# Kernel optimization log

Hardware: AMD Instinct MI355X
Metric: run time of the kernel (lower is better)

The kernel has to match this reference:

```python
import jax, jax.numpy as jnp
import numpy as np

T, B, N, DEG, F_IN, H, C = 48, 32, 96, 8, 16, 128, 500
E = B * N * DEG          # edges per timestep (already batch-offset within [0, B*N))
M = T * B * N            # total nodes across all timesteps
EPS = 1e-5               # BatchNorm eps


def setup_inputs() -> dict:
    key = jax.random.key(0)
    ks = jax.random.split(key, 24)
    rn = lambda k, s: jax.random.normal(k, s, dtype=jnp.float32) * 0.05
    return {
        "x": jax.random.normal(ks[0], (T, B * N, F_IN), dtype=jnp.float32),
        "edge_index": jax.random.randint(ks[1], (T, 2, E), 0, B * N, dtype=jnp.int32),
        "gcn_w0": rn(ks[2], (F_IN, H)),
        "gcn_w12": rn(ks[3], (2, H, H)),
        "gcn_b": rn(ks[4], (3, H)),
        "bn_gamma": jnp.ones((3, H), dtype=jnp.float32),
        "bn_beta": jnp.zeros((3, H), dtype=jnp.float32),
        "bn_mean": rn(ks[5], (3, H)),
        "bn_var": jax.random.uniform(ks[6], (3, H), minval=0.5, maxval=1.5, dtype=jnp.float32),
        "lstm_wih0": rn(ks[7], (2, 4 * H, H)),
        "lstm_whh0": rn(ks[8], (2, 4 * H, H)),
        "lstm_bih0": rn(ks[9], (2, 4 * H)),
        "lstm_bhh0": rn(ks[10], (2, 4 * H)),
        "lstm_wih1": rn(ks[11], (2, 4 * H, 2 * H)),
        "lstm_whh1": rn(ks[12], (2, 4 * H, H)),
        "lstm_bih1": rn(ks[13], (2, 4 * H)),
        "lstm_bhh1": rn(ks[14], (2, 4 * H)),
        "attn_w1": rn(ks[15], (2 * H, H)),
        "attn_b1": rn(ks[16], (H,)),
        "attn_w2": rn(ks[17], (H, 1)),
        "attn_b2": rn(ks[18], (1,)),
        "fc1_w": rn(ks[19], (2 * H, H)),
        "fc1_b": rn(ks[20], (H,)),
        "fc2_w": rn(ks[21], (H, C)),
        "fc2_b": rn(ks[22], (C,)),
    }


def _lstm_dir(x, wih, whh, bih, bhh):
    # x: [T, B, I]; PyTorch gate order i, f, g, o
    pre = jnp.einsum('tbi,gi->tbg', x, wih) + bih  # input projection hoisted out of scan
    h0 = jnp.zeros((x.shape[1], whh.shape[1]), x.dtype)

    def step(carry, p):
        h, c = carry
        g = p + h @ whh.T + bhh
        i, f, gg, o = jnp.split(g, 4, axis=-1)
        c = jax.nn.sigmoid(f) * c + jax.nn.sigmoid(i) * jnp.tanh(gg)
        h = jax.nn.sigmoid(o) * jnp.tanh(c)
        return (h, c), h

    _, hs = jax.lax.scan(step, (h0, h0), pre)
    return hs  # [T, B, Hh]


def _bilstm(x, wih, whh, bih, bhh):
    fwd = _lstm_dir(x, wih[0], whh[0], bih[0], bhh[0])
    bwd = _lstm_dir(x[::-1], wih[1], whh[1], bih[1], bhh[1])[::-1]
    return jnp.concatenate([fwd, bwd], axis=-1)  # [T, B, 2H]


def reference(x, edge_index, gcn_w0, gcn_w12, gcn_b,
              bn_gamma, bn_beta, bn_mean, bn_var,
              lstm_wih0, lstm_whh0, lstm_bih0, lstm_bhh0,
              lstm_wih1, lstm_whh1, lstm_bih1, lstm_bhh1,
              attn_w1, attn_b1, attn_w2, attn_b2,
              fc1_w, fc1_b, fc2_w, fc2_b):
    # Fold timesteps into one big node set by offsetting indices by t*B*N
    off = (jnp.arange(T, dtype=jnp.int32) * (B * N))[:, None]
    src = (edge_index[:, 0] + off).reshape(-1)
    dst = (edge_index[:, 1] + off).reshape(-1)

    # GCN symmetric norm with self-loops: deg counts incoming edges + self-loop
    deg = jax.ops.segment_sum(jnp.ones_like(src, dtype=x.dtype), dst, num_segments=M) + 1.0
    dinv = jax.lax.rsqrt(deg)
    enorm = (dinv[src] * dinv[dst])[:, None]   # per-edge norm
    self_norm = (1.0 / deg)[:, None]           # self-loop norm

    h = x.reshape(M, F_IN)
    for l in range(3):
        W = gcn_w0 if l == 0 else gcn_w12[l - 1]
        hw = h @ W  # GCNConv applies linear first
        z = jax.ops.segment_sum(hw[src] * enorm, dst, num_segments=M) + hw * self_norm + gcn_b[l]
        # BatchNorm1d eval-mode (running stats), then ReLU, residual if shapes match
        z = (z - bn_mean[l]) * (bn_gamma[l] * jax.lax.rsqrt(bn_var[l] + EPS)) + bn_beta[l]
        z = jax.nn.relu(z)
        h = z + h if l > 0 else z  # dropout is identity in eval

    # global_mean_pool per graph (fixed N nodes per graph)
    emb = h.reshape(T, B, N, H).mean(axis=2)  # [T, B, H]

    out1 = _bilstm(emb, lstm_wih0, lstm_whh0, lstm_bih0, lstm_bhh0)
    out2 = _bilstm(out1, lstm_wih1, lstm_whh1, lstm_bih1, lstm_bhh1)
    lstm_out = out2.transpose(1, 0, 2)  # [B, T, 2H]

    a = jnp.tanh(lstm_out @ attn_w1 + attn_b1) @ attn_w2 + attn_b2  # [B, T, 1]
    w = jax.nn.softmax(a, axis=1)
    ws = jnp.sum(lstm_out * w, axis=1)  # [B, 2H]

    y = jax.nn.relu(ws @ fc1_w + fc1_b) @ fc2_w + fc2_b
    return jax.nn.log_softmax(y, axis=1)
```

## Files before the change

kernel.cpp:

```cpp
#include <hip/hip_runtime.h>

#define T_ 48
#define B_ 32
#define N_ 96
#define E_ 24576
#define BN_ (B_*N_)
#define M_ (T_*BN_)
#define FIN_ 16
#define H_ 128
#define C_ 500
#define TE_ (T_*E_)
#define EPS_ 1e-5f

typedef _Float16 f16x8 __attribute__((ext_vector_type(8)));
typedef float    f32x4 __attribute__((ext_vector_type(4)));
typedef _Float16 half2v __attribute__((ext_vector_type(2)));

__device__ __forceinline__ ushort f2h(float f) {
    _Float16 h = (_Float16)f;
    union { _Float16 h; ushort u; } v;
    v.h = h;
    return v.u;
}
__device__ __forceinline__ float h2f(ushort u) {
    union { ushort u; _Float16 h; } v;
    v.u = u;
    return (float)v.h;
}
__device__ __forceinline__ half2v pkfma(unsigned int v, unsigned int w, half2v acc) {
#if __has_builtin(__builtin_elementwise_fma)
    return __builtin_elementwise_fma(__builtin_bit_cast(half2v, v),
                                     __builtin_bit_cast(half2v, w), acc);
#else
    half2v hv = __builtin_bit_cast(half2v, v);
    half2v wv = __builtin_bit_cast(half2v, w);
    acc[0] += hv[0]*wv[0];
    acc[1] += hv[1]*wv[1];
    return acc;
#endif
}
__device__ __forceinline__ float dot2pk(unsigned int hbits, unsigned int wbits, float acc) {
#if __has_builtin(__builtin_amdgcn_fdot2)
    return __builtin_amdgcn_fdot2(__builtin_bit_cast(half2v, hbits),
                                  __builtin_bit_cast(half2v, wbits), acc, false);
#else
    half2v hv = __builtin_bit_cast(half2v, hbits);
    half2v wv = __builtin_bit_cast(half2v, wbits);
    acc = fmaf((float)hv[0], (float)wv[0], acc);
    acc = fmaf((float)hv[1], (float)wv[1], acc);
    return acc;
#endif
}
__device__ __forceinline__ float sigm(float x) {
    return 1.f / (1.f + __expf(-x));
}
__device__ __forceinline__ float ftanh(float x) {
    x = fminf(15.f, fmaxf(-15.f, x));
    float e = __expf(2.f * x);
    return (e - 1.f) / (e + 1.f);
}

__global__ __launch_bounds__(1024) void csr_build_k(
    const int* __restrict__ ei, int* __restrict__ csr_off,
    unsigned int* __restrict__ csr_pk, float* __restrict__ dinv)
{
    int t = blockIdx.x;
    int tid = threadIdx.x;
    __shared__ int cnt[BN_];
    __shared__ int cur[BN_];
    __shared__ int scanbuf[1024];
    __shared__ unsigned int pk[E_];

    #pragma unroll
    for (int i = 0; i < 3; i++) cnt[tid + i*1024] = 0;
    __syncthreads();

    const int* srcp = ei + ((long)t*2+0)*E_;
    const int* dstp = ei + ((long)t*2+1)*E_;
    #pragma unroll
    for (int i = 0; i < E_/1024; i++)
        atomicAdd(&cnt[dstp[tid + i*1024]], 1);
    __syncthreads();

    int n0 = tid*3;
    int a = cnt[n0], b = cnt[n0+1], c = cnt[n0+2];
    int tot = a + b + c;
    scanbuf[tid] = tot;
    __syncthreads();
    for (int d = 1; d < 1024; d <<= 1) {
        int add = (tid >= d) ? scanbuf[tid-d] : 0;
        __syncthreads();
        scanbuf[tid] += add;
        __syncthreads();
    }
    int excl = scanbuf[tid] - tot;
    cur[n0] = excl; cur[n0+1] = excl + a; cur[n0+2] = excl + a + b;
    int gbase = t*BN_, ebase = t*E_;
    csr_off[gbase+n0]   = ebase + excl;
    csr_off[gbase+n0+1] = ebase + excl + a;
    csr_off[gbase+n0+2] = ebase + excl + a + b;
    dinv[gbase+n0]   = rsqrtf((float)a + 1.f);
    dinv[gbase+n0+1] = rsqrtf((float)b + 1.f);
    dinv[gbase+n0+2] = rsqrtf((float)c + 1.f);
    if (t == T_-1 && tid == 0) csr_off[M_] = TE_;
    __syncthreads();

    #pragma unroll
    for (int i = 0; i < E_/1024; i++) {
        int e = tid + i*1024;
        int s = srcp[e], d = dstp[e];
        int pos = atomicAdd(&cur[d], 1);
        float w = rsqrtf((float)cnt[s] + 1.f) * rsqrtf((float)cnt[d] + 1.f);
        pk[pos] = (unsigned int)s | ((unsigned int)f2h(w) << 16);
    }
    __syncthreads();

    uint4* dpk = (uint4*)(csr_pk + ebase);
    const uint4* spk = (const uint4*)pk;
    #pragma unroll
    for (int i = 0; i < E_/4096; i++)
        dpk[tid + i*1024] = spk[tid + i*1024];
}

#define WPREP_TOTAL (384+1024+4096+16384+16384+65536+65536+131072+262144)
__global__ void wprep_k(
    const float* __restrict__ gcn_b, const float* __restrict__ gam,
    const float* __restrict__ bet, const float* __restrict__ mu,
    const float* __restrict__ var,
    float* __restrict__ bn_sc, float* __restrict__ bn_sh,
    const float* __restrict__ bih0, const float* __restrict__ bhh0,
    float* __restrict__ bias0,
    const float* __restrict__ bih1, const float* __restrict__ bhh1,
    float* __restrict__ bias1,
    const float* __restrict__ gcn_w0, const float* __restrict__ gcn_w12,
    ushort* __restrict__ w0t, ushort* __restrict__ w1t, ushort* __restrict__ w2t,
    const float* __restrict__ whh0, const float* __restrict__ whh1,
    unsigned int* __restrict__ wpk0, unsigned int* __restrict__ wpk1,
    const float* __restrict__ wih0, const float* __restrict__ wih1,
    ushort* __restrict__ wih0b, ushort* __restrict__ wih1b)
{
    int i = blockIdx.x * blockDim.x + threadIdx.x;
    if (i >= WPREP_TOTAL) return;
    if (i < 384) {
        float sc = gam[i] * rsqrtf(var[i] + EPS_);
        bn_sc[i] = sc;
        bn_sh[i] = gcn_b[i]*sc + bet[i] - mu[i]*sc;
        return;
    }
    i -= 384;
    if (i < 1024) {
        bias0[i] = bih0[i] + bhh0[i];
        bias1[i] = bih1[i] + bhh1[i];
        return;
    }
    i -= 1024;
    if (i < 4096) {
        int e = i & 7, lane = (i >> 3) & 63, ct = i >> 9;
        int k = (lane >> 4)*8 + e;
        int c = ct*16 + (lane & 15);
        w0t[i] = (k < 16) ? f2h(gcn_w0[k*128 + c]) : (ushort)0;
        return;
    }
    i -= 4096;
    if (i < 16384) {
        int e = i & 7, lane = (i >> 3) & 63, kk = (i >> 9) & 3, ct = i >> 11;
        int k = kk*32 + (lane >> 4)*8 + e;
        int c = ct*16 + (lane & 15);
        w1t[i] = f2h(gcn_w12[k*128 + c]);
        return;
    }
    i -= 16384;
    if (i < 16384) {
        int e = i & 7, lane = (i >> 3) & 63, kk = (i >> 9) & 3, ct = i >> 11;
        int k = kk*32 + (lane >> 4)*8 + e;
        int c = ct*16 + (lane & 15);
        w2t[i] = f2h(gcn_w12[16384 + k*128 + c]);
        return;
    }
    i -= 16384;
    if (i < 65536) {
        int dir = i >> 15, r = i & 32767;
        int ab = r >> 14, r2 = r & 16383;
        int q = r2 >> 8, tidw = r2 & 255;
        int hh = tidw >> 1, gp = tidw & 1;
        int g = (2*gp + ab)*128 + hh;
        const float* wr = whh0 + ((long)(dir*512 + g))*128 + 2*q;
        wpk0[i] = (unsigned int)f2h(wr[0]) | ((unsigned int)f2h(wr[1]) << 16);
        return;
    }
    i -= 65536;
    if (i < 65536) {
        int dir = i >> 15, r = i & 32767;
        int ab = r >> 14, r2 = r & 16383;
        int q = r2 >> 8, tidw = r2 & 255;
        int hh = tidw >> 1, gp = tidw & 1;
        int g = (2*gp + ab)*128 + hh;
        const float* wr = whh1 + ((long)(dir*512 + g))*128 + 2*q;
        wpk1[i] = (unsigned int)f2h(wr[0]) | ((unsigned int)f2h(wr[1]) << 16);
        return;
    }
    i -= 65536;
    if (i < 131072) {
        int dir = i >> 16, r = i & 0xFFFF;
        int nt = r >> 11, kk = (r >> 9) & 3, lane = (r >> 3) & 63, e = r & 7;
        int n = nt*16 + (lane & 15);
        int k = kk*32 + (lane >> 4)*8 + e;
        wih0b[i] = f2h(wih0[((long)dir*512 + n)*128 + k]);
        return;
    }
    i -= 131072;
    {
        int dir = i >> 17, r = i & 0x1FFFF;
        int nt = r >> 12, kk = (r >> 9) & 7, lane = (r >> 3) & 63, e = r & 7;
        int n = nt*16 + (lane & 15);
        int k = kk*32 + (lane >> 4)*8 + e;
        wih1b[i] = f2h(wih1[((long)dir*512 + n)*256 + k]);
    }
}


__global__ __launch_bounds__(256) void gather128_k(
    const ushort* __restrict__ h, ushort* __restrict__ out,
    const int* __restrict__ csr_off, const unsigned int* __restrict__ csr_pk,
    const float* __restrict__ dinv)
{
    int nb = gridDim.x;
    int chunk = nb >> 3;
    int bswz = (blockIdx.x & 7) * chunk + (blockIdx.x >> 3);
    int wv = threadIdx.x >> 6;
    int nodeA = __builtin_amdgcn_readfirstlane(bswz*8 + wv*2);
    int tbase = (nodeA / BN_) * BN_;
    int lane = threadIdx.x & 63;
    int l2 = lane * 2;
    int e00 = __builtin_amdgcn_readfirstlane(csr_off[nodeA]);
    int e01 = __builtin_amdgcn_readfirstlane(csr_off[nodeA+1]);
    int e11 = __builtin_amdgcn_readfirstlane(csr_off[nodeA+2]);
    int dA = e01 - e00, dB = e11 - e01;
    unsigned int mypkA = (lane < dA) ? csr_pk[e00 + lane] : 0u;
    unsigned int mypkB = (lane < dB) ? csr_pk[e01 + lane] : 0u;
    float dvA = dinv[nodeA], dvB = dinv[nodeA+1];
    unsigned int selfA = *(const unsigned int*)(h + (size_t)nodeA*128 + l2);
    unsigned int selfB = *(const unsigned int*)(h + (size_t)(nodeA+1)*128 + l2);

    ushort swA = f2h(dvA * dvA), swB = f2h(dvB * dvB);
    half2v spA = __builtin_bit_cast(half2v, (unsigned int)(swA * 0x10001u));
    half2v spB = __builtin_bit_cast(half2v, (unsigned int)(swB * 0x10001u));
    half2v a0 = __builtin_bit_cast(half2v, selfA);
    a0[0] *= spA[0]; a0[1] *= spA[1];
    half2v b0 = __builtin_bit_cast(half2v, selfB);
    b0[0] *= spB[0]; b0[1] *= spB[1];
    half2v a1 = {(_Float16)0.f, (_Float16)0.f}, a2 = a1, a3 = a1;
    half2v b1 = a1, b2 = a1, b3 = a1;

    int cA = (dA < 64) ? dA : 64;
    int cB = (dB < 64) ? dB : 64;
    int cA4 = cA & ~3, cB4 = cB & ~3;
    int cm = (cA4 > cB4) ? cA4 : cB4;
    for (int j = 0; j < cm; j += 4) {
        unsigned int pA0, pA1, pA2, pA3, vA0, vA1, vA2, vA3;
        unsigned int pB0, pB1, pB2, pB3, vB0, vB1, vB2, vB3;
        bool qA = (j < cA4), qB = (j < cB4);
        if (qA) {
            pA0 = (unsigned int)__builtin_amdgcn_readlane((int)mypkA, j+0);
            pA1 = (unsigned int)__builtin_amdgcn_readlane((int)mypkA, j+1);
            pA2 = (unsigned int)__builtin_amdgcn_readlane((int)mypkA, j+2);
            pA3 = (unsigned int)__builtin_amdgcn_readlane((int)mypkA, j+3);
            vA0 = *(const unsigned int*)(h + (size_t)(tbase + (int)(pA0 & 0xffffu))*128 + l2);
            vA1 = *(const unsigned int*)(h + (size_t)(tbase + (int)(pA1 & 0xffffu))*128 + l2);
            vA2 = *(const unsigned int*)(h + (size_t)(tbase + (int)(pA2 & 0xffffu))*128 + l2);
            vA3 = *(const unsigned int*)(h + (size_t)(tbase + (int)(pA3 & 0xffffu))*128 + l2);
        }
        if (qB) {
            pB0 = (unsigned int)__builtin_amdgcn_readlane((int)mypkB, j+0);
            pB1 = (unsigned int)__builtin_amdgcn_readlane((int)mypkB, j+1);
            pB2 = (unsigned int)__builtin_amdgcn_readlane((int)mypkB, j+2);
            pB3 = (unsigned int)__builtin_amdgcn_readlane((int)mypkB, j+3);
            vB0 = *(const unsigned int*)(h + (size_t)(tbase + (int)(pB0 & 0xffffu))*128 + l2);
            vB1 = *(const unsigned int*)(h + (size_t)(tbase + (int)(pB1 & 0xffffu))*128 + l2);
            vB2 = *(const unsigned int*)(h + (size_t)(tbase + (int)(pB2 & 0xffffu))*128 + l2);
            vB3 = *(const unsigned int*)(h + (size_t)(tbase + (int)(pB3 & 0xffffu))*128 + l2);
        }
        if (qA) {
            a0 = pkfma(vA0, (pA0 >> 16) * 0x10001u, a0);
            a1 = pkfma(vA1, (pA1 >> 16) * 0x10001u, a1);
            a2 = pkfma(vA2, (pA2 >> 16) * 0x10001u, a2);
            a3 = pkfma(vA3, (pA3 >> 16) * 0x10001u, a3);
        }
        if (qB) {
            b0 = pkfma(vB0, (pB0 >> 16) * 0x10001u, b0);
            b1 = pkfma(vB1, (pB1 >> 16) * 0x10001u, b1);
            b2 = pkfma(vB2, (pB2 >> 16) * 0x10001u, b2);
            b3 = pkfma(vB3, (pB3 >> 16) * 0x10001u, b3);
        }
    }
    for (int j = cA4; j < cA; j++) {
        unsigned int pk0 = (unsigned int)__builtin_amdgcn_readlane((int)mypkA, j);
        unsigned int v = *(const unsigned int*)(h + (size_t)(tbase + (int)(pk0 & 0xffffu))*128 + l2);
        a0 = pkfma(v, (pk0 >> 16) * 0x10001u, a0);
    }
    for (int j = cB4; j < cB; j++) {
        unsigned int pk0 = (unsigned int)__builtin_amdgcn_readlane((int)mypkB, j);
        unsigned int v = *(const unsigned int*)(h + (size_t)(tbase + (int)(pk0 & 0xffffu))*128 + l2);
        b0 = pkfma(v, (pk0 >> 16) * 0x10001u, b0);
    }
    for (int jj = e00 + 64; jj < e01; jj++) {
        unsigned int pk0 = __builtin_amdgcn_readfirstlane(csr_pk[jj]);
        unsigned int v = *(const unsigned int*)(h + (size_t)(tbase + (int)(pk0 & 0xffffu))*128 + l2);
        a0 = pkfma(v, (pk0 >> 16) * 0x10001u, a0);
    }
    for (int jj = e01 + 64; jj < e11; jj++) {
        unsigned int pk0 = __builtin_amdgcn_readfirstlane(csr_pk[jj]);
        unsigned int v = *(const unsigned int*)(h + (size_t)(tbase + (int)(pk0 & 0xffffu))*128 + l2);
        b0 = pkfma(v, (pk0 >> 16) * 0x10001u, b0);
    }
    float ra0 = ((float)a0[0] + (float)a1[0]) + ((float)a2[0] + (float)a3[0]);
    float ra1 = ((float)a0[1] + (float)a1[1]) + ((float)a2[1] + (float)a3[1]);
    float rb0 = ((float)b0[0] + (float)b1[0]) + ((float)b2[0] + (float)b3[0]);
    float rb1 = ((float)b0[1] + (float)b1[1]) + ((float)b2[1] + (float)b3[1]);
    *(unsigned int*)(out + (size_t)nodeA*128 + l2) =
        (unsigned int)f2h(ra0) | ((unsigned int)f2h(ra1) << 16);
    *(unsigned int*)(out + (size_t)(nodeA+1)*128 + l2) =
        (unsigned int)f2h(rb0) | ((unsigned int)f2h(rb1) << 16);
}

__global__ __launch_bounds__(256) void gcn0_k(
    const float* __restrict__ x, const ushort* __restrict__ Wt,
    ushort* __restrict__ Cout,
    const int* __restrict__ csr_off, const unsigned int* __restrict__ csr_pk,
    const float* __restrict__ dinv,
    const float* __restrict__ bnsc, const float* __restrict__ bnsh)
{
    __shared__ ushort agg[64][32];
    __shared__ ushort cl[64][136];
    int tid = threadIdx.x;
    int nl = tid >> 2;
    int fq = tid & 3;
    int f0 = fq*4;
    int node = blockIdx.x*64 + nl;
    int tbase = (node / BN_) * BN_;
    float dv = dinv[node];
    float4 sv = *(const float4*)(x + (long)node*16 + f0);
    float s = dv*dv;
    float a0 = sv.x*s, a1 = sv.y*s, a2 = sv.z*s, a3 = sv.w*s;
    int e0 = csr_off[node], e1 = csr_off[node+1];
    int j = e0;
    for (; j + 4 <= e1; j += 4) {
        unsigned int p0 = csr_pk[j], p1 = csr_pk[j+1], p2 = csr_pk[j+2], p3 = csr_pk[j+3];
        int s0 = tbase + (int)(p0 & 0xffffu), s1 = tbase + (int)(p1 & 0xffffu);
        int s2 = tbase + (int)(p2 & 0xffffu), s3 = tbase + (int)(p3 & 0xffffu);
        float w0 = h2f((ushort)(p0 >> 16)), w1 = h2f((ushort)(p1 >> 16));
        float w2 = h2f((ushort)(p2 >> 16)), w3 = h2f((ushort)(p3 >> 16));
        float4 v0 = *(const float4*)(x + (long)s0*16 + f0);
        float4 v1 = *(const float4*)(x + (long)s1*16 + f0);
        float4 v2 = *(const float4*)(x + (long)s2*16 + f0);
        float4 v3 = *(const float4*)(x + (long)s3*16 + f0);
        a0 += v0.x*w0 + v1.x*w1 + v2.x*w2 + v3.x*w3;
        a1 += v0.y*w0 + v1.y*w1 + v2.y*w2 + v3.y*w3;
        a2 += v0.z*w0 + v1.z*w1 + v2.z*w2 + v3.z*w3;
        a3 += v0.w*w0 + v1.w*w1 + v2.w*w2 + v3.w*w3;
    }
    for (; j < e1; j++) {
        unsigned int pk0 = csr_pk[j];
        int sc = tbase + (int)(pk0 & 0xffffu);
        float en = h2f((ushort)(pk0 >> 16));
        float4 v = *(const float4*)(x + (long)sc*16 + f0);
        a0 += v.x*en; a1 += v.y*en; a2 += v.z*en; a3 += v.w*en;
    }
    agg[nl][f0+0] = f2h(a0);
    agg[nl][f0+1] = f2h(a1);
    agg[nl][f0+2] = f2h(a2);
    agg[nl][f0+3] = f2h(a3);
    agg[nl][16+f0+0] = 0;
    agg[nl][16+f0+1] = 0;
    agg[nl][16+f0+2] = 0;
    agg[nl][16+f0+3] = 0;
    __syncthreads();

    int w = tid >> 6, lane = tid & 63;
    int l16 = lane & 15, lh = lane >> 4;
    f16x8 af = *reinterpret_cast<const f16x8*>(&agg[w*16 + l16][lh*8]);
    f32x4 acc[8];
    #pragma unroll
    for (int i = 0; i < 8; i++) acc[i] = (f32x4){0.f, 0.f, 0.f, 0.f};
    #pragma unroll
    for (int ct = 0; ct < 8; ct++) {
        f16x8 bfr = *reinterpret_cast<const f16x8*>(&Wt[((long)ct*64 + lane)*8]);
        acc[ct] = __builtin_amdgcn_mfma_f32_16x16x32_f16(af, bfr, acc[ct], 0, 0, 0);
    }

    #pragma unroll
    for (int ct = 0; ct < 8; ct++) {
        int col = ct*16 + l16;
        float sc = bnsc[col], sh = bnsh[col];
        #pragma unroll
        for (int r = 0; r < 4; r++) {
            int rl = w*16 + lh*4 + r;
            float v = acc[ct][r] * sc + sh;
            cl[rl][col] = f2h(fmaxf(v, 0.f));
        }
    }
    __syncthreads();
    long rowblock = (long)blockIdx.x * 64;
    #pragma unroll
    for (int it = 0; it < 4; it++) {
        int ss = it*256 + tid;
        int rl = ss >> 4, c8 = (ss & 15) * 8;
        uint4 v = *(const uint4*)&cl[rl][c8];
        *(uint4*)&Cout[(rowblock + rl)*128 + c8] = v;
    }
}

template<int K, bool HASRES>
__global__ __launch_bounds__(256) void mm_mfma_k(
    const ushort* __restrict__ A, const ushort* __restrict__ Wt,
    ushort* __restrict__ Cout,
    const float* __restrict__ bnsc, const float* __restrict__ bnsh,
    const ushort* __restrict__ resid)
{
    constexpr int KST = (K >= 32) ? (K/32) : 1;
    int tid = threadIdx.x;
    int w = tid >> 6, lane = tid & 63;
    int l16 = lane & 15, lh = lane >> 4;
    int row0 = blockIdx.x * 64 + w * 16;
    __shared__ ushort cl[64][136];

    f32x4 acc[8];
    #pragma unroll
    for (int i = 0; i < 8; i++) acc[i] = (f32x4){0.f, 0.f, 0.f, 0.f};

    #pragma unroll
    for (int kk = 0; kk < KST; kk++) {
        int ka = kk*32 + lh*8;
        f16x8 af;
        bool valid = (K >= 32) || (ka < K);
        if (valid) {
            af = *reinterpret_cast<const f16x8*>(&A[(long)(row0 + l16)*K + ka]);
        } else {
            #pragma unroll
            for (int e = 0; e < 8; e++) af[e] = (_Float16)0.f;
        }
        #pragma unroll
        for (int ct = 0; ct < 8; ct++) {
            f16x8 bfr = *reinterpret_cast<const f16x8*>(
                &Wt[(((long)ct*KST + kk)*64 + lane)*8]);
            acc[ct] = __builtin_amdgcn_mfma_f32_16x16x32_f16(af, bfr, acc[ct], 0, 0, 0);
        }
    }

    #pragma unroll
    for (int ct = 0; ct < 8; ct++) {
        int col = ct*16 + l16;
        float sc = bnsc[col], sh = bnsh[col];
        #pragma unroll
        for (int r = 0; r < 4; r++) {
            int rl = w*16 + lh*4 + r;
            float v = acc[ct][r] * sc + sh;
            cl[rl][col] = f2h(fmaxf(v, 0.f));
        }
    }
    __syncthreads();
    long rowblock = (long)blockIdx.x * 64;
    #pragma unroll
    for (int it = 0; it < 4; it++) {
        int s = it*256 + tid;
        int rl = s >> 4, c8 = (s & 15) * 8;
        uint4 v = *(const uint4*)&cl[rl][c8];
        if (HASRES) {
            uint4 rv = *(const uint4*)&resid[(rowblock + rl)*128 + c8];
            half2v* vv = (half2v*)&v;
            const half2v* rr = (const half2v*)&rv;
            vv[0] += rr[0]; vv[1] += rr[1]; vv[2] += rr[2]; vv[3] += rr[3];
        }
        *(uint4*)&Cout[(rowblock + rl)*128 + c8] = v;
    }
}

template<int K>
__global__ __launch_bounds__(256) void mm_pre_k(
    const ushort* __restrict__ A, const ushort* __restrict__ Wt_all,
    float* __restrict__ Cout_all, const float* __restrict__ bias_all)
{
    constexpr int KST = K/32;
    int dir = blockIdx.z;
    const ushort* Wt = Wt_all + (size_t)dir * 512 * K;
    float* Cout = Cout_all + (size_t)dir * T_ * B_ * 512;
    const float* bias = bias_all + dir * 512;

    int tid = threadIdx.x;
    int w = tid >> 6, lane = tid & 63;
    int l16 = lane & 15, lh = lane >> 4;
    int row0 = blockIdx.x * 64 + w * 16;
    int nt0 = blockIdx.y * 8;

    f32x4 acc[8];
    #pragma unroll
    for (int i = 0; i < 8; i++) acc[i] = (f32x4){0.f, 0.f, 0.f, 0.f};

    #pragma unroll
    for (int kk = 0; kk < KST; kk++) {
        int ka = kk*32 + lh*8;
        f16x8 af = *reinterpret_cast<const f16x8*>(&A[(long)(row0 + l16)*K + ka]);
        #pragma unroll
        for (int ct = 0; ct < 8; ct++) {
            f16x8 bfr = *reinterpret_cast<const f16x8*>(
                &Wt[(((long)(nt0 + ct)*KST + kk)*64 + lane)*8]);
            acc[ct] = __builtin_amdgcn_mfma_f32_16x16x32_f16(af, bfr, acc[ct], 0, 0, 0);
        }
    }

    #pragma unroll
    for (int ct = 0; ct < 8; ct++) {
        int col = (nt0 + ct)*16 + l16;
        float bv = bias[col];
        int gate = col >> 7, hh = col & 127;
        int colp = (gate & 1)*256 + hh*2 + (gate >> 1);
        #pragma unroll
        for (int r = 0; r < 4; r++) {
            int row = row0 + lh*4 + r;
            Cout[(long)row*512 + colp] = acc[ct][r] + bv;
        }
    }
}


__global__ void meanpool_k(const ushort* __restrict__ h, ushort* __restrict__ embb) {
    int row = blockIdx.x;
    int t = row / B_, b = row - t*B_;
    int hh = threadIdx.x;
    const ushort* base = h + ((long)t*BN_ + b*N_)*H_ + hh;
    float acc = 0.f;
    for (int n = 0; n < N_; n++) acc += h2f(base[(long)n*H_]);
    embb[(long)row*H_ + hh] = f2h(acc * (1.f / N_));
}

__global__ __launch_bounds__(256) void lstm_scan_k(
    const float* __restrict__ pre,
    const unsigned int* __restrict__ wpkbuf,
    float* __restrict__ out,
    ushort* __restrict__ outb)
{
    int dir = blockIdx.x >> 5;
    int b   = blockIdx.x & 31;
    int tid = threadIdx.x;
    int gp  = tid & 1;
    int hh  = tid >> 1;

    __shared__ ushort hbuf[2][H_];
    ((ushort*)hbuf)[tid] = 0;
    float creg = 0.f;

    const unsigned int* wpA = wpkbuf + ((long)dir*2 + 0)*64*256;
    const unsigned int* wpB = wpkbuf + ((long)dir*2 + 1)*64*256;
    unsigned int wA[64], wB[64];
    #pragma unroll
    for (int q = 0; q < 64; q++) {
        wA[q] = wpA[q*256 + tid];
        wB[q] = wpB[q*256 + tid];
    }

    const float* pred = pre + (long)dir * T_ * B_ * 512;
    int t = dir ? (T_ - 1) : 0;
    int tstep = dir ? -1 : 1;
    float pvA = pred[(((long)t*B_ + b)*2 + 0)*256 + tid];
    float pvB = pred[(((long)t*B_ + b)*2 + 1)*256 + tid];
    __syncthreads();

    for (int st = 0; st < T_; st++) {
        int tn = t + tstep;
        tn = (tn < 0) ? 0 : ((tn >= T_) ? T_ - 1 : tn);
        float pvAn = pred[(((long)tn*B_ + b)*2 + 0)*256 + tid];
        float pvBn = pred[(((long)tn*B_ + b)*2 + 1)*256 + tid];

        const uint4* h4 = (const uint4*)hbuf[st & 1];
        float a0 = pvA, a1 = 0.f, a2 = 0.f, a3 = 0.f;
        float c0 = pvB, c1 = 0.f, c2 = 0.f, c3 = 0.f;
        #pragma unroll
        for (int jj = 0; jj < 16; jj++) {
            uint4 hv = h4[jj];
            a0 = dot2pk(hv.x, wA[jj*4+0], a0);
            a1 = dot2pk(hv.y, wA[jj*4+1], a1);
            a2 = dot2pk(hv.z, wA[jj*4+2], a2);
            a3 = dot2pk(hv.w, wA[jj*4+3], a3);
            c0 = dot2pk(hv.x, wB[jj*4+0], c0);
            c1 = dot2pk(hv.y, wB[jj*4+1], c1);
            c2 = dot2pk(hv.z, wB[jj*4+2], c2);
            c3 = dot2pk(hv.w, wB[jj*4+3], c3);
        }
        float sA = (a0 + a1) + (a2 + a3);
        float sB = (c0 + c1) + (c2 + c3);
        float oA = __shfl_xor(sA, 1, 64);
        float oB = __shfl_xor(sB, 1, 64);
        float ig = gp ? oA : sA;
        float fg = gp ? oB : sB;
        float gg = gp ? sA : oA;
        float og = gp ? sB : oB;
        float c = sigm(fg) * creg + sigm(ig) * ftanh(gg);
        float h = sigm(og) * ftanh(c);
        creg = c;
        if (gp == 0) {
            hbuf[(st + 1) & 1][hh] = f2h(h);
            long orow = ((long)t*B_ + b)*256 + dir*H_ + hh;
            if (out)  out[orow] = h;
            if (outb) outb[orow] = f2h(h);
        }
        __syncthreads();
        pvA = pvAn; pvB = pvBn;
        t = tn;
    }
}


__global__ __launch_bounds__(128) void attn_a_k(
    const ushort* __restrict__ out2, const float* __restrict__ w1,
    const float* __restrict__ b1, const float* __restrict__ w2,
    const float* __restrict__ b2v, float* __restrict__ a)
{
    int row = blockIdx.x;
    int j = threadIdx.x;
    const ushort* xr = out2 + (long)row * 256;
    float acc = b1[j];
    for (int k = 0; k < 256; k++) acc += h2f(xr[k]) * w1[k*128 + j];
    float u = tanhf(acc) * w2[j];
    __shared__ float red[128];
    red[j] = u;
    __syncthreads();
    for (int d = 64; d > 0; d >>= 1) {
        if (j < d) red[j] += red[j + d];
        __syncthreads();
    }
    if (j == 0) {
        int t = row / B_, b = row - t*B_;
        a[b*T_ + t] = red[0] + b2v[0];
    }
}

__global__ __launch_bounds__(256) void attn_pool_k(
    const ushort* __restrict__ out2, const float* __restrict__ a,
    float* __restrict__ wsv)
{
    int b = blockIdx.x;
    __shared__ float w[T_];
    if (threadIdx.x == 0) {
        float m = -1e30f;
        for (int t = 0; t < T_; t++) m = fmaxf(m, a[b*T_ + t]);
        float s = 0.f;
        for (int t = 0; t < T_; t++) { float e = __expf(a[b*T_ + t] - m); w[t] = e; s += e; }
        float inv = 1.f / s;
        for (int t = 0; t < T_; t++) w[t] *= inv;
    }
    __syncthreads();
    int h2 = threadIdx.x;
    float acc = 0.f;
    for (int t = 0; t < T_; t++) acc += w[t] * h2f(out2[((long)t*B_ + b)*256 + h2]);
    wsv[b*256 + h2] = acc;
}


__global__ __launch_bounds__(512) void head_k(
    const float* __restrict__ wsv, const float* __restrict__ w1,
    const float* __restrict__ b1, const float* __restrict__ w2,
    const float* __restrict__ b2, float* __restrict__ outp)
{
    int b = blockIdx.x;
    int tid = threadIdx.x;
    __shared__ float r[128];
    __shared__ float y[C_];
    __shared__ float red[512];
    if (tid < 128) {
        float acc = b1[tid];
        for (int k = 0; k < 256; k++) acc += wsv[b*256 + k] * w1[k*128 + tid];
        r[tid] = fmaxf(acc, 0.f);
    }
    __syncthreads();
    for (int c = tid; c < C_; c += 512) {
        float acc = b2[c];
        for (int k = 0; k < 128; k++) acc += r[k] * w2[k*C_ + c];
        y[c] = acc;
    }
    __syncthreads();
    float m = -1e30f;
    for (int c = tid; c < C_; c += 512) m = fmaxf(m, y[c]);
    red[tid] = m;
    __syncthreads();
    for (int d = 256; d > 0; d >>= 1) {
        if (tid < d) red[tid] = fmaxf(red[tid], red[tid + d]);
        __syncthreads();
    }
    m = red[0];
    __syncthreads();
    float s = 0.f;
    for (int c = tid; c < C_; c += 512) s += __expf(y[c] - m);
    red[tid] = s;
    __syncthreads();
    for (int d = 256; d > 0; d >>= 1) {
        if (tid < d) red[tid] += red[tid + d];
        __syncthreads();
    }
    float lse = m + logf(red[0]);
    for (int c = tid; c < C_; c += 512) outp[(long)b*C_ + c] = y[c] - lse;
}


extern "C" void kernel_launch(void* const* d_in, const int* in_sizes, int n_in,
                              void* d_out, int out_size, void* d_ws, size_t ws_size,
                              hipStream_t stream) {
    const float* x        = (const float*)d_in[0];
    const int*   ei       = (const int*)d_in[1];
    const float* gcn_w0   = (const float*)d_in[2];
    const float* gcn_w12  = (const float*)d_in[3];
    const float* gcn_b    = (const float*)d_in[4];
    const float* bn_gamma = (const float*)d_in[5];
    const float* bn_beta  = (const float*)d_in[6];
    const float* bn_mean  = (const float*)d_in[7];
    const float* bn_var   = (const float*)d_in[8];
    const float* wih0     = (const float*)d_in[9];
    const float* whh0     = (const float*)d_in[10];
    const float* bih0     = (const float*)d_in[11];
    const float* bhh0     = (const float*)d_in[12];
    const float* wih1     = (const float*)d_in[13];
    const float* whh1     = (const float*)d_in[14];
    const float* bih1     = (const float*)d_in[15];
    const float* bhh1     = (const float*)d_in[16];
    const float* attn_w1  = (const float*)d_in[17];
    const float* attn_b1  = (const float*)d_in[18];
    const float* attn_w2  = (const float*)d_in[19];
    const float* attn_b2  = (const float*)d_in[20];
    const float* fc1_w    = (const float*)d_in[21];
    const float* fc1_b    = (const float*)d_in[22];
    const float* fc2_w    = (const float*)d_in[23];
    const float* fc2_b    = (const float*)d_in[24];

    char* p = (char*)d_ws;
    auto alloc = [&](size_t bytes) {
        void* r = (void*)p;
        p += (bytes + 255) & ~(size_t)255;
        return r;
    };
    ushort* aggbuf = (ushort*)alloc((size_t)M_*H_*2);
    ushort* hbA    = (ushort*)alloc((size_t)M_*H_*2);
    ushort* hbB    = (ushort*)alloc((size_t)M_*H_*2);
    float* dinv    = (float*)alloc((size_t)M_*4);
    int*   csr_off = (int*)  alloc((size_t)(M_+1)*4);
    unsigned int* csr_pk = (unsigned int*)alloc((size_t)TE_*4);
    float* bn_sc   = (float*)alloc(384*4);
    float* bn_sh   = (float*)alloc(384*4);
    float* bias0   = (float*)alloc(1024*4);
    float* bias1   = (float*)alloc(1024*4);
    ushort* w0t    = (ushort*)alloc((size_t)4096*2);
    ushort* w1t    = (ushort*)alloc((size_t)16384*2);
    ushort* w2t    = (ushort*)alloc((size_t)16384*2);
    unsigned int* wpk0 = (unsigned int*)alloc((size_t)2*64*512*4);
    unsigned int* wpk1 = (unsigned int*)alloc((size_t)2*64*512*4);
    ushort* wih0b  = (ushort*)alloc((size_t)2*512*128*2);
    ushort* wih1b  = (ushort*)alloc((size_t)2*512*256*2);
    ushort* embb   = (ushort*)alloc((size_t)T_*B_*H_*2);
    float* pre     = (float*)alloc((size_t)2*T_*B_*512*4);
    ushort* out1b  = (ushort*)alloc((size_t)T_*B_*256*2);
    ushort* out2b  = (ushort*)alloc((size_t)T_*B_*256*2);
    float* attn_av = (float*)alloc((size_t)B_*T_*4);
    float* wsv     = (float*)alloc((size_t)B_*256*4);

    csr_build_k<<<T_, 1024, 0, stream>>>(ei, csr_off, csr_pk, dinv);

    wprep_k<<<(WPREP_TOTAL+255)/256, 256, 0, stream>>>(
        gcn_b, bn_gamma, bn_beta, bn_mean, bn_var, bn_sc, bn_sh,
        bih0, bhh0, bias0, bih1, bhh1, bias1,
        gcn_w0, gcn_w12, w0t, w1t, w2t,
        whh0, whh1, wpk0, wpk1,
        wih0, wih1, wih0b, wih1b);

    gcn0_k<<<M_/64, 256, 0, stream>>>(x, w0t, hbA, csr_off, csr_pk, dinv,
                                      bn_sc + 0, bn_sh + 0);
    gather128_k<<<M_/8, 256, 0, stream>>>(hbA, aggbuf, csr_off, csr_pk, dinv);
    mm_mfma_k<128, true><<<M_/64, 256, 0, stream>>>(aggbuf, w1t, hbB,
                                                    bn_sc + 128, bn_sh + 128, hbA);
    gather128_k<<<M_/8, 256, 0, stream>>>(hbB, aggbuf, csr_off, csr_pk, dinv);
    mm_mfma_k<128, true><<<M_/64, 256, 0, stream>>>(aggbuf, w2t, hbA,
                                                    bn_sc + 256, bn_sh + 256, hbB);

    meanpool_k<<<T_*B_, 128, 0, stream>>>(hbA, embb);

    mm_pre_k<128><<<dim3((T_*B_)/64, 4, 2), 256, 0, stream>>>(embb, wih0b, pre, bias0);
    lstm_scan_k<<<64, 256, 0, stream>>>(pre, wpk0, nullptr, out1b);

    mm_pre_k<256><<<dim3((T_*B_)/64, 4, 2), 256, 0, stream>>>(out1b, wih1b, pre, bias1);
    lstm_scan_k<<<64, 256, 0, stream>>>(pre, wpk1, nullptr, out2b);

    attn_a_k<<<T_*B_, 128, 0, stream>>>(out2b, attn_w1, attn_b1, attn_w2, attn_b2, attn_av);
    attn_pool_k<<<B_, 256, 0, stream>>>(out2b, attn_av, wsv);

    head_k<<<B_, 512, 0, stream>>>(wsv, fc1_w, fc1_b, fc2_w, fc2_b, (float*)d_out);
}
```

Baseline: 318.2 us.

## Fuse GCN neighbor gather with MFMA linear, BN, ReLU and residual

Merges the separate gather kernel and MFMA matmul kernel for GCN layers 1 and 2 into one kernel. Each block gathers 64 nodes' aggregated features into LDS, then runs the MFMA projection, BatchNorm, ReLU and residual add directly from shared memory. This removes the global round trip of the aggregation buffer and two launches per layer. In exchange, each block now covers 64 nodes with 8 serial gather passes, so the grid is 8x smaller and there may be less latency hiding during the irregular gather phase.

```diff
diff --git a/kernel.cpp b/kernel.cpp
--- a/kernel.cpp
+++ b/kernel.cpp
@@ -218,109 +218,158 @@
     }
 }
 
-
-__global__ __launch_bounds__(256) void gather128_k(
-    const ushort* __restrict__ h, ushort* __restrict__ out,
+__global__ __launch_bounds__(256) void gcn_layer_k(
+    const ushort* __restrict__ h, const ushort* __restrict__ Wt,
+    ushort* __restrict__ Cout,
     const int* __restrict__ csr_off, const unsigned int* __restrict__ csr_pk,
-    const float* __restrict__ dinv)
-{
+    const float* __restrict__ dinv,
+    const float* __restrict__ bnsc, const float* __restrict__ bnsh)
+{
+    __shared__ ushort agg[64][136];
     int nb = gridDim.x;
     int chunk = nb >> 3;
     int bswz = (blockIdx.x & 7) * chunk + (blockIdx.x >> 3);
+    int base = bswz * 64;
+    int tbase = (base / BN_) * BN_;
     int wv = threadIdx.x >> 6;
-    int nodeA = __builtin_amdgcn_readfirstlane(bswz*8 + wv*2);
-    int tbase = (nodeA / BN_) * BN_;
     int lane = threadIdx.x & 63;
     int l2 = lane * 2;
-    int e00 = __builtin_amdgcn_readfirstlane(csr_off[nodeA]);
-    int e01 = __builtin_amdgcn_readfirstlane(csr_off[nodeA+1]);
-    int e11 = __builtin_amdgcn_readfirstlane(csr_off[nodeA+2]);
-    int dA = e01 - e00, dB = e11 - e01;
-    unsigned int mypkA = (lane < dA) ? csr_pk[e00 + lane] : 0u;
-    unsigned int mypkB = (lane < dB) ? csr_pk[e01 + lane] : 0u;
-    float dvA = dinv[nodeA], dvB = dinv[nodeA+1];
-    unsigned int selfA = *(const unsigned int*)(h + (size_t)nodeA*128 + l2);
-    unsigned int selfB = *(const unsigned int*)(h + (size_t)(nodeA+1)*128 + l2);
-
-    ushort swA = f2h(dvA * dvA), swB = f2h(dvB * dvB);
-    half2v spA = __builtin_bit_cast(half2v, (unsigned int)(swA * 0x10001u));
-    half2v spB = __builtin_bit_cast(half2v, (unsigned int)(swB * 0x10001u));
-    half2v a0 = __builtin_bit_cast(half2v, selfA);
-    a0[0] *= spA[0]; a0[1] *= spA[1];
-    half2v b0 = __builtin_bit_cast(half2v, selfB);
-    b0[0] *= spB[0]; b0[1] *= spB[1];
-    half2v a1 = {(_Float16)0.f, (_Float16)0.f}, a2 = a1, a3 = a1;
-    half2v b1 = a1, b2 = a1, b3 = a1;
-
-    int cA = (dA < 64) ? dA : 64;
-    int cB = (dB < 64) ? dB : 64;
-    int cA4 = cA & ~3, cB4 = cB & ~3;
-    int cm = (cA4 > cB4) ? cA4 : cB4;
-    for (int j = 0; j < cm; j += 4) {
-        unsigned int pA0, pA1, pA2, pA3, vA0, vA1, vA2, vA3;
-        unsigned int pB0, pB1, pB2, pB3, vB0, vB1, vB2, vB3;
-        bool qA = (j < cA4), qB = (j < cB4);
-        if (qA) {
-            pA0 = (unsigned int)__builtin_amdgcn_readlane((int)mypkA, j+0);
-            pA1 = (unsigned int)__builtin_amdgcn_readlane((int)mypkA, j+1);
-            pA2 = (unsigned int)__builtin_amdgcn_readlane((int)mypkA, j+2);
-            pA3 = (unsigned int)__builtin_amdgcn_readlane((int)mypkA, j+3);
-            vA0 = *(const unsigned int*)(h + (size_t)(tbase + (int)(pA0 & 0xffffu))*128 + l2);
-            vA1 = *(const unsigned int*)(h + (size_t)(tbase + (int)(pA1 & 0xffffu))*128 + l2);
-            vA2 = *(const unsigned int*)(h + (size_t)(tbase + (int)(pA2 & 0xffffu))*128 + l2);
-            vA3 = *(const unsigned int*)(h + (size_t)(tbase + (int)(pA3 & 0xffffu))*128 + l2);
-        }
-        if (qB) {
-            pB0 = (unsigned int)__builtin_amdgcn_readlane((int)mypkB, j+0);
-            pB1 = (unsigned int)__builtin_amdgcn_readlane((int)mypkB, j+1);
-            pB2 = (unsigned int)__builtin_amdgcn_readlane((int)mypkB, j+2);
-            pB3 = (unsigned int)__builtin_amdgcn_readlane((int)mypkB, j+3);
-            vB0 = *(const unsigned int*)(h + (size_t)(tbase + (int)(pB0 & 0xffffu))*128 + l2);
-            vB1 = *(const unsigned int*)(h + (size_t)(tbase + (int)(pB1 & 0xffffu))*128 + l2);
-            vB2 = *(const unsigned int*)(h + (size_t)(tbase + (int)(pB2 & 0xffffu))*128 + l2);
-            vB3 = *(const unsigned int*)(h + (size_t)(tbase + (int)(pB3 & 0xffffu))*128 + l2);
-        }
-        if (qA) {
-            a0 = pkfma(vA0, (pA0 >> 16) * 0x10001u, a0);
-            a1 = pkfma(vA1, (pA1 >> 16) * 0x10001u, a1);
-            a2 = pkfma(vA2, (pA2 >> 16) * 0x10001u, a2);
-            a3 = pkfma(vA3, (pA3 >> 16) * 0x10001u, a3);
-        }
-        if (qB) {
-            b0 = pkfma(vB0, (pB0 >> 16) * 0x10001u, b0);
-            b1 = pkfma(vB1, (pB1 >> 16) * 0x10001u, b1);
-            b2 = pkfma(vB2, (pB2 >> 16) * 0x10001u, b2);
-            b3 = pkfma(vB3, (pB3 >> 16) * 0x10001u, b3);
-        }
-    }
-    for (int j = cA4; j < cA; j++) {
-        unsigned int pk0 = (unsigned int)__builtin_amdgcn_readlane((int)mypkA, j);
-        unsigned int v = *(const unsigned int*)(h + (size_t)(tbase + (int)(pk0 & 0xffffu))*128 + l2);
-        a0 = pkfma(v, (pk0 >> 16) * 0x10001u, a0);
-    }
-    for (int j = cB4; j < cB; j++) {
-        unsigned int pk0 = (unsigned int)__builtin_amdgcn_readlane((int)mypkB, j);
-        unsigned int v = *(const unsigned int*)(h + (size_t)(tbase + (int)(pk0 & 0xffffu))*128 + l2);
-        b0 = pkfma(v, (pk0 >> 16) * 0x10001u, b0);
-    }
-    for (int jj = e00 + 64; jj < e01; jj++) {
-        unsigned int pk0 = __builtin_amdgcn_readfirstlane(csr_pk[jj]);
-        unsigned int v = *(const unsigned int*)(h + (size_t)(tbase + (int)(pk0 & 0xffffu))*128 + l2);
-        a0 = pkfma(v, (pk0 >> 16) * 0x10001u, a0);
-    }
-    for (int jj = e01 + 64; jj < e11; jj++) {
-        unsigned int pk0 = __builtin_amdgcn_readfirstlane(csr_pk[jj]);
-        unsigned int v = *(const unsigned int*)(h + (size_t)(tbase + (int)(pk0 & 0xffffu))*128 + l2);
-        b0 = pkfma(v, (pk0 >> 16) * 0x10001u, b0);
-    }
-    float ra0 = ((float)a0[0] + (float)a1[0]) + ((float)a2[0] + (float)a3[0]);
-    float ra1 = ((float)a0[1] + (float)a1[1]) + ((float)a2[1] + (float)a3[1]);
-    float rb0 = ((float)b0[0] + (float)b1[0]) + ((float)b2[0] + (float)b3[0]);
-    float rb1 = ((float)b0[1] + (float)b1[1]) + ((float)b2[1] + (float)b3[1]);
-    *(unsigned int*)(out + (size_t)nodeA*128 + l2) =
-        (unsigned int)f2h(ra0) | ((unsigned int)f2h(ra1) << 16);
-    *(unsigned int*)(out + (size_t)(nodeA+1)*128 + l2) =
-        (unsigned int)f2h(rb0) | ((unsigned int)f2h(rb1) << 16);
+
+    for (int pass = 0; pass < 8; pass++) {
+        int nodeA = __builtin_amdgcn_readfirstlane(base + pass*8 + wv*2);
+        int e00 = __builtin_amdgcn_readfirstlane(csr_off[nodeA]);
+        int e01 = __builtin_amdgcn_readfirstlane(csr_off[nodeA+1]);
+        int e11 = __builtin_amdgcn_readfirstlane(csr_off[nodeA+2]);
+        int dA = e01 - e00, dB = e11 - e01;
+        unsigned int mypkA = (lane < dA) ? csr_pk[e00 + lane] : 0u;
+        unsigned int mypkB = (lane < dB) ? csr_pk[e01 + lane] : 0u;
+        float dvA = dinv[nodeA], dvB = dinv[nodeA+1];
+        unsigned int selfA = *(const unsigned int*)(h + (size_t)nodeA*128 + l2);
+        unsigned int selfB = *(const unsigned int*)(h + (size_t)(nodeA+1)*128 + l2);
+
+        ushort swA = f2h(dvA * dvA), swB = f2h(dvB * dvB);
+        half2v spA = __builtin_bit_cast(half2v, (unsigned int)(swA * 0x10001u));
+        half2v spB = __builtin_bit_cast(half2v, (unsigned int)(swB * 0x10001u));
+        half2v a0 = __builtin_bit_cast(half2v, selfA);
+        a0[0] *= spA[0]; a0[1] *= spA[1];
+        half2v b0 = __builtin_bit_cast(half2v, selfB);
+        b0[0] *= spB[0]; b0[1] *= spB[1];
+        half2v a1 = {(_Float16)0.f, (_Float16)0.f}, a2 = a1, a3 = a1;
+        half2v b1 = a1, b2 = a1, b3 = a1;
+
+        int cA = (dA < 64) ? dA : 64;
+        int cB = (dB < 64) ? dB : 64;
+        int cA4 = cA & ~3, cB4 = cB & ~3;
+        int cm = (cA4 > cB4) ? cA4 : cB4;
+        for (int j = 0; j < cm; j += 4) {
+            unsigned int pA0, pA1, pA2, pA3, vA0, vA1, vA2, vA3;
+            unsigned int pB0, pB1, pB2, pB3, vB0, vB1, vB2, vB3;
+            bool qA = (j < cA4), qB = (j < cB4);
+            if (qA) {
+                pA0 = (unsigned int)__builtin_amdgcn_readlane((int)mypkA, j+0);
+                pA1 = (unsigned int)__builtin_amdgcn_readlane((int)mypkA, j+1);
+                pA2 = (unsigned int)__builtin_amdgcn_readlane((int)mypkA, j+2);
+                pA3 = (unsigned int)__builtin_amdgcn_readlane((int)mypkA, j+3);
+                vA0 = *(const unsigned int*)(h + (size_t)(tbase + (int)(pA0 & 0xffffu))*128 + l2);
+                vA1 = *(const unsigned int*)(h + (size_t)(tbase + (int)(pA1 & 0xffffu))*128 + l2);
+                vA2 = *(const unsigned int*)(h + (size_t)(tbase + (int)(pA2 & 0xffffu))*128 + l2);
+                vA3 = *(const unsigned int*)(h + (size_t)(tbase + (int)(pA3 & 0xffffu))*128 + l2);
+            }
+            if (qB) {
+                pB0 = (unsigned int)__builtin_amdgcn_readlane((int)mypkB, j+0);
+                pB1 = (unsigned int)__builtin_amdgcn_readlane((int)mypkB, j+1);
+                pB2 = (unsigned int)__builtin_amdgcn_readlane((int)mypkB, j+2);
+                pB3 = (unsigned int)__builtin_amdgcn_readlane((int)mypkB, j+3);
+                vB0 = *(const unsigned int*)(h + (size_t)(tbase + (int)(pB0 & 0xffffu))*128 + l2);
+                vB1 = *(const unsigned int*)(h + (size_t)(tbase + (int)(pB1 & 0xffffu))*128 + l2);
+                vB2 = *(const unsigned int*)(h + (size_t)(tbase + (int)(pB2 & 0xffffu))*128 + l2);
+                vB3 = *(const unsigned int*)(h + (size_t)(tbase + (int)(pB3 & 0xffffu))*128 + l2);
+            }
+            if (qA) {
+                a0 = pkfma(vA0, (pA0 >> 16) * 0x10001u, a0);
+                a1 = pkfma(vA1, (pA1 >> 16) * 0x10001u, a1);
+                a2 = pkfma(vA2, (pA2 >> 16) * 0x10001u, a2);
+                a3 = pkfma(vA3, (pA3 >> 16) * 0x10001u, a3);
+            }
+            if (qB) {
+                b0 = pkfma(vB0, (pB0 >> 16) * 0x10001u, b0);
+                b1 = pkfma(vB1, (pB1 >> 16) * 0x10001u, b1);
+                b2 = pkfma(vB2, (pB2 >> 16) * 0x10001u, b2);
+                b3 = pkfma(vB3, (pB3 >> 16) * 0x10001u, b3);
+            }
+        }
+        for (int j = cA4; j < cA; j++) {
+            unsigned int pk0 = (unsigned int)__builtin_amdgcn_readlane((int)mypkA, j);
+            unsigned int v = *(const unsigned int*)(h + (size_t)(tbase + (int)(pk0 & 0xffffu))*128 + l2);
+            a0 = pkfma(v, (pk0 >> 16) * 0x10001u, a0);
+        }
+        for (int j = cB4; j < cB; j++) {
+            unsigned int pk0 = (unsigned int)__builtin_amdgcn_readlane((int)mypkB, j);
+            unsigned int v = *(const unsigned int*)(h + (size_t)(tbase + (int)(pk0 & 0xffffu))*128 + l2);
+            b0 = pkfma(v, (pk0 >> 16) * 0x10001u, b0);
+        }
+        for (int jj = e00 + 64; jj < e01; jj++) {
+            unsigned int pk0 = __builtin_amdgcn_readfirstlane(csr_pk[jj]);
+            unsigned int v = *(const unsigned int*)(h + (size_t)(tbase + (int)(pk0 & 0xffffu))*128 + l2);
+            a0 = pkfma(v, (pk0 >> 16) * 0x10001u, a0);
+        }
+        for (int jj = e01 + 64; jj < e11; jj++) {
+            unsigned int pk0 = __builtin_amdgcn_readfirstlane(csr_pk[jj]);
+            unsigned int v = *(const unsigned int*)(h + (size_t)(tbase + (int)(pk0 & 0xffffu))*128 + l2);
+            b0 = pkfma(v, (pk0 >> 16) * 0x10001u, b0);
+        }
+        float ra0 = ((float)a0[0] + (float)a1[0]) + ((float)a2[0] + (float)a3[0]);
+        float ra1 = ((float)a0[1] + (float)a1[1]) + ((float)a2[1] + (float)a3[1]);
+        float rb0 = ((float)b0[0] + (float)b1[0]) + ((float)b2[0] + (float)b3[0]);
+        float rb1 = ((float)b0[1] + (float)b1[1]) + ((float)b2[1] + (float)b3[1]);
+        int nlA = nodeA - base;
+        *(unsigned int*)&agg[nlA][l2] =
+            (unsigned int)f2h(ra0) | ((unsigned int)f2h(ra1) << 16);
+        *(unsigned int*)&agg[nlA+1][l2] =
+            (unsigned int)f2h(rb0) | ((unsigned int)f2h(rb1) << 16);
+    }
+    __syncthreads();
+
+    int l16 = lane & 15, lh = lane >> 4;
+    f32x4 acc[8];
+    #pragma unroll
+    for (int i = 0; i < 8; i++) acc[i] = (f32x4){0.f, 0.f, 0.f, 0.f};
+    #pragma unroll
+    for (int kk = 0; kk < 4; kk++) {
+        f16x8 af = *reinterpret_cast<const f16x8*>(&agg[wv*16 + l16][kk*32 + lh*8]);
+        #pragma unroll
+        for (int ct = 0; ct < 8; ct++) {
+            f16x8 bfr = *reinterpret_cast<const f16x8*>(
+                &Wt[(((long)ct*4 + kk)*64 + lane)*8]);
+            acc[ct] = __builtin_amdgcn_mfma_f32_16x16x32_f16(af, bfr, acc[ct], 0, 0, 0);
+        }
+    }
+    __syncthreads();
+
+    #pragma unroll
+    for (int ct = 0; ct < 8; ct++) {
+        int col = ct*16 + l16;
+        float sc = bnsc[col], sh = bnsh[col];
+        #pragma unroll
+        for (int r = 0; r < 4; r++) {
+            int rl = wv*16 + lh*4 + r;
+            float v = acc[ct][r] * sc + sh;
+            agg[rl][col] = f2h(fmaxf(v, 0.f));
+        }
+    }
+    __syncthreads();
+    long rowblock = (long)base;
+    #pragma unroll
+    for (int it = 0; it < 4; it++) {
+        int s = it*256 + threadIdx.x;
+        int rl = s >> 4, c8 = (s & 15) * 8;
+        uint4 v = *(const uint4*)&agg[rl][c8];
+        uint4 rv = *(const uint4*)&h[(rowblock + rl)*128 + c8];
+        half2v* vv = (half2v*)&v;
+        const half2v* rr = (const half2v*)&rv;
+        vv[0] += rr[0]; vv[1] += rr[1]; vv[2] += rr[2]; vv[3] += rr[3];
+        *(uint4*)&Cout[(rowblock + rl)*128 + c8] = v;
+    }
 }
 
 __global__ __launch_bounds__(256) void gcn0_k(
@@ -410,71 +459,6 @@
     }
 }
 
-template<int K, bool HASRES>
-__global__ __launch_bounds__(256) void mm_mfma_k(
-    const ushort* __restrict__ A, const ushort* __restrict__ Wt,
-    ushort* __restrict__ Cout,
-    const float* __restrict__ bnsc, const float* __restrict__ bnsh,
-    const ushort* __restrict__ resid)
-{
-    constexpr int KST = (K >= 32) ? (K/32) : 1;
-    int tid = threadIdx.x;
-    int w = tid >> 6, lane = tid & 63;
-    int l16 = lane & 15, lh = lane >> 4;
-    int row0 = blockIdx.x * 64 + w * 16;
-    __shared__ ushort cl[64][136];
-
-    f32x4 acc[8];
-    #pragma unroll
-    for (int i = 0; i < 8; i++) acc[i] = (f32x4){0.f, 0.f, 0.f, 0.f};
-
-    #pragma unroll
-    for (int kk = 0; kk < KST; kk++) {
-        int ka = kk*32 + lh*8;
-        f16x8 af;
-        bool valid = (K >= 32) || (ka < K);
-        if (valid) {
-            af = *reinterpret_cast<const f16x8*>(&A[(long)(row0 + l16)*K + ka]);
-        } else {
-            #pragma unroll
-            for (int e = 0; e < 8; e++) af[e] = (_Float16)0.f;
-        }
-        #pragma unroll
-        for (int ct = 0; ct < 8; ct++) {
-            f16x8 bfr = *reinterpret_cast<const f16x8*>(
-                &Wt[(((long)ct*KST + kk)*64 + lane)*8]);
-            acc[ct] = __builtin_amdgcn_mfma_f32_16x16x32_f16(af, bfr, acc[ct], 0, 0, 0);
-        }
-    }
-
-    #pragma unroll
-    for (int ct = 0; ct < 8; ct++) {
-        int col = ct*16 + l16;
-        float sc = bnsc[col], sh = bnsh[col];
-        #pragma unroll
-        for (int r = 0; r < 4; r++) {
-            int rl = w*16 + lh*4 + r;
-            float v = acc[ct][r] * sc + sh;
-            cl[rl][col] = f2h(fmaxf(v, 0.f));
-        }
-    }
-    __syncthreads();
-    long rowblock = (long)blockIdx.x * 64;
-    #pragma unroll
-    for (int it = 0; it < 4; it++) {
-        int s = it*256 + tid;
-        int rl = s >> 4, c8 = (s & 15) * 8;
-        uint4 v = *(const uint4*)&cl[rl][c8];
-        if (HASRES) {
-            uint4 rv = *(const uint4*)&resid[(rowblock + rl)*128 + c8];
-            half2v* vv = (half2v*)&v;
-            const half2v* rr = (const half2v*)&rv;
-            vv[0] += rr[0]; vv[1] += rr[1]; vv[2] += rr[2]; vv[3] += rr[3];
-        }
-        *(uint4*)&Cout[(rowblock + rl)*128 + c8] = v;
-    }
-}
-
 template<int K>
 __global__ __launch_bounds__(256) void mm_pre_k(
     const ushort* __restrict__ A, const ushort* __restrict__ Wt_all,
@@ -736,7 +720,6 @@
         p += (bytes + 255) & ~(size_t)255;
         return r;
     };
-    ushort* aggbuf = (ushort*)alloc((size_t)M_*H_*2);
     ushort* hbA    = (ushort*)alloc((size_t)M_*H_*2);
     ushort* hbB    = (ushort*)alloc((size_t)M_*H_*2);
     float* dinv    = (float*)alloc((size_t)M_*4);
@@ -771,12 +754,10 @@
 
     gcn0_k<<<M_/64, 256, 0, stream>>>(x, w0t, hbA, csr_off, csr_pk, dinv,
                                       bn_sc + 0, bn_sh + 0);
-    gather128_k<<<M_/8, 256, 0, stream>>>(hbA, aggbuf, csr_off, csr_pk, dinv);
-    mm_mfma_k<128, true><<<M_/64, 256, 0, stream>>>(aggbuf, w1t, hbB,
-                                                    bn_sc + 128, bn_sh + 128, hbA);
-    gather128_k<<<M_/8, 256, 0, stream>>>(hbB, aggbuf, csr_off, csr_pk, dinv);
-    mm_mfma_k<128, true><<<M_/64, 256, 0, stream>>>(aggbuf, w2t, hbA,
-                                                    bn_sc + 256, bn_sh + 256, hbB);
+    gcn_layer_k<<<M_/64, 256, 0, stream>>>(hbA, w1t, hbB, csr_off, csr_pk, dinv,
+                                           bn_sc + 128, bn_sh + 128);
+    gcn_layer_k<<<M_/64, 256, 0, stream>>>(hbB, w2t, hbA, csr_off, csr_pk, dinv,
+                                           bn_sc + 256, bn_sh + 256);
 
     meanpool_k<<<T_*B_, 128, 0, stream>>>(hbA, embb);
 
```

Result: faster. 301.4 us (-5.3%).
